# Optimization experiments

Hardware: AMD Instinct MI355X
Metric: run time of the kernel (lower is better)

## Reference

```python
import jax, jax.numpy as jnp
import numpy as np

N_NODES = 50000
N_EDGES = 400000
IN_DIM = 64
HID = 128
HEADS = 4
NEG_SLOPE = 0.2


def gat_conv(x, src, dst, W, a_src, a_dst, b, heads, out_ch, concat):
    N = x.shape[0]
    h = (x @ W).reshape(N, heads, out_ch)                 # [N,H,C]
    alpha_s = jnp.einsum('nhc,hc->nh', h, a_src)          # [N,H]
    alpha_d = jnp.einsum('nhc,hc->nh', h, a_dst)
    e = jax.nn.leaky_relu(alpha_s[src] + alpha_d[dst], NEG_SLOPE)  # [E,H]
    m = jax.ops.segment_max(e, dst, num_segments=N)
    m = jnp.where(jnp.isfinite(m), m, 0.0)
    ex = jnp.exp(e - m[dst])
    s = jax.ops.segment_sum(ex, dst, num_segments=N)
    alpha = ex / s[dst]                                   # segment softmax over incoming edges
    out = jax.ops.segment_sum(h[src] * alpha[:, :, None], dst, num_segments=N)  # [N,H,C]
    out = out.reshape(N, heads * out_ch) if concat else out.mean(axis=1)
    return out + b


def setup_inputs() -> dict:
    key = jax.random.key(0)
    ks = jax.random.split(key, 20)
    g = lambda i, shape, sc: (jax.random.normal(ks[i], shape, jnp.float32) * sc)
    x = g(0, (N_NODES, IN_DIM), 1.0)
    edge_index = jax.random.randint(ks[1], (2, N_EDGES), 0, N_NODES, dtype=jnp.int32)
    d = {
        'x': x, 'edge_index': edge_index,
        'W1': g(2, (IN_DIM, HEADS * HID), 0.1), 'a_src1': g(3, (HEADS, HID), 0.1), 'a_dst1': g(4, (HEADS, HID), 0.1), 'b1': jnp.zeros((HEADS * HID,), jnp.float32),
        'W2': g(5, (HEADS * HID, HEADS * HID), 0.05), 'a_src2': g(6, (HEADS, HID), 0.1), 'a_dst2': g(7, (HEADS, HID), 0.1), 'b2': jnp.zeros((HEADS * HID,), jnp.float32),
        'W3': g(8, (HEADS * HID, HID), 0.05), 'a_src3': g(9, (1, HID), 0.1), 'a_dst3': g(10, (1, HID), 0.1), 'b3': jnp.zeros((HID,), jnp.float32),
        'fc1_w': g(11, (HID, HID // 2), 0.1), 'fc1_b': jnp.zeros((HID // 2,), jnp.float32),
        'fc2_w': g(12, (HID // 2, 1), 0.1), 'fc2_b': jnp.zeros((1,), jnp.float32),
    }
    return d


def reference(x, edge_index, W1, a_src1, a_dst1, b1, W2, a_src2, a_dst2, b2, W3, a_src3, a_dst3, b3, fc1_w, fc1_b, fc2_w, fc2_b):
    N = x.shape[0]
    loop = jnp.arange(N, dtype=edge_index.dtype)
    src = jnp.concatenate([edge_index[0], loop])  # PyG GATConv adds self-loops by default
    dst = jnp.concatenate([edge_index[1], loop])
    h = jax.nn.elu(gat_conv(x, src, dst, W1, a_src1, a_dst1, b1, HEADS, HID, True))
    h = jax.nn.elu(gat_conv(h, src, dst, W2, a_src2, a_dst2, b2, HEADS, HID, True))
    h = jax.nn.elu(gat_conv(h, src, dst, W3, a_src3, a_dst3, b3, 1, HID, False))
    h = jax.nn.relu(h @ fc1_w + fc1_b)
    return jax.nn.sigmoid(h @ fc2_w + fc2_b)  # [N, 1]
```

## Files before the change

### kernel.cpp

```cpp
#include <hip/hip_runtime.h>
#include <math.h>

typedef __attribute__((ext_vector_type(8))) short short8;
typedef __attribute__((ext_vector_type(4))) float f32x4;
typedef unsigned short u16;
typedef unsigned int u32;

__device__ inline u16 f2b(float f) {
  u32 u = __float_as_uint(f);
  return (u16)((u + 0x7FFFu + ((u >> 16) & 1u)) >> 16);
}
__device__ inline float b2f(u16 b) { return __uint_as_float((u32)b << 16); }
__device__ inline float lrelu(float v) { return v > 0.f ? v : 0.2f * v; }
__device__ inline float elu1(float v) { return v > 0.f ? v : __expf(v) - 1.f; }

__device__ inline void gld_lds16(const void* g, void* l) {
  __builtin_amdgcn_global_load_lds((const __attribute__((address_space(1))) void*)g,
                                   (__attribute__((address_space(3))) void*)l, 16, 0, 0);
}

__global__ void fused_prep(const float* __restrict__ x, u16* __restrict__ xb, int NX,
                           const float* __restrict__ W1, u16* __restrict__ Wt1,
                           const float* __restrict__ W2, u16* __restrict__ Wt2,
                           const float* __restrict__ W3, u16* __restrict__ Wt3,
                           const int* __restrict__ ei, int E0, int ET,
                           int* __restrict__ deg) {
  int i = blockIdx.x * blockDim.x + threadIdx.x;
  if (i < NX) {
    xb[i] = f2b(x[i]);
    return;
  }
  i -= NX;
  if (i < 64 * 512) {
    int k = i / 512, n = i % 512;
    Wt1[n * 64 + k] = f2b(W1[i]);
    return;
  }
  i -= 64 * 512;
  if (i < 512 * 512) {
    int k = i / 512, n = i % 512;
    Wt2[n * 512 + k] = f2b(W2[i]);
    return;
  }
  i -= 512 * 512;
  if (i < 512 * 128) {
    int k = i / 128, n = i % 128;
    Wt3[n * 512 + k] = f2b(W3[i]);
    return;
  }
  i -= 512 * 128;
  if (i < ET) {
    int d = (i < E0) ? ei[E0 + i] : (i - E0);
    atomicAdd(&deg[d], 1);
  }
}

__global__ __launch_bounds__(256) void gemm_bf16_gat(
    const u16* __restrict__ A, const u16* __restrict__ Bt, u16* __restrict__ Hb,
    const float* __restrict__ a_src, const float* __restrict__ a_dst,
    float* __restrict__ aS, float* __restrict__ aD, int M, int HC, int K, int Hh,
    int gy, int nStrips) {
  int mIdx, nIdx;
  if (nStrips == 4) {
    int l = blockIdx.x;
    int xcd = l & 7, k = l >> 3;
    nIdx = k & 3;
    mIdx = xcd + 8 * (k >> 2);
    if (mIdx >= gy) return;
  } else {
    mIdx = blockIdx.x;
    nIdx = 0;
  }
  __shared__ u16 As[128 * 32];
  __shared__ u16 Bs[128 * 32];
  __shared__ float sRed[2][2][128];
  const int tid = threadIdx.x;
  const int w = tid >> 6, lane = tid & 63;
  const int wm = w >> 1, wn = w & 1;
  const int q = lane >> 4, l15 = lane & 15;
  const int nBase = nIdx * 128;
  const int mBase = mIdx * 128;
  const int h = nBase >> 7;
  const int srow = lane >> 2;
  const int skc = (lane & 3) * 8;

  f32x4 acc[4][4];
#pragma unroll
  for (int i = 0; i < 4; ++i)
#pragma unroll
    for (int j = 0; j < 4; ++j) acc[i][j] = (f32x4){0.f, 0.f, 0.f, 0.f};

  for (int k0 = 0; k0 < K; k0 += 32) {
#pragma unroll
    for (int r = 0; r < 2; ++r) {
      int lrow = w * 32 + r * 16 + srow;
      int ga = mBase + lrow;
      if (ga >= M) ga = M - 1;
      gld_lds16(A + (size_t)ga * K + k0 + skc, &As[(w * 32 + r * 16) * 32]);
      int gb = nBase + lrow;
      gld_lds16(Bt + (size_t)gb * K + k0 + skc, &Bs[(w * 32 + r * 16) * 32]);
    }
    __syncthreads();
    short8 af[4], bf[4];
#pragma unroll
    for (int i = 0; i < 4; ++i)
      af[i] = *(const short8*)&As[(wm * 64 + i * 16 + l15) * 32 + q * 8];
#pragma unroll
    for (int j = 0; j < 4; ++j)
      bf[j] = *(const short8*)&Bs[(wn * 64 + j * 16 + l15) * 32 + q * 8];
#pragma unroll
    for (int i = 0; i < 4; ++i)
#pragma unroll
      for (int j = 0; j < 4; ++j)
        acc[i][j] = __builtin_amdgcn_mfma_f32_16x16x32_bf16(af[i], bf[j], acc[i][j], 0, 0, 0);
    __syncthreads();
  }

  float asv[4], adv[4];
#pragma unroll
  for (int j = 0; j < 4; ++j) {
    int cw = wn * 64 + j * 16 + l15;
    asv[j] = a_src[h * 128 + cw];
    adv[j] = a_dst[h * 128 + cw];
  }
#pragma unroll
  for (int mi = 0; mi < 4; ++mi) {
#pragma unroll
    for (int r = 0; r < 4; ++r) {
      int row = mBase + wm * 64 + mi * 16 + q * 4 + r;
      float s = 0.f, d = 0.f;
#pragma unroll
      for (int j = 0; j < 4; ++j) {
        float v = acc[mi][j][r];
        s = fmaf(v, asv[j], s);
        d = fmaf(v, adv[j], d);
        if (row < M) Hb[(size_t)row * HC + nBase + wn * 64 + j * 16 + l15] = f2b(v);
      }
#pragma unroll
      for (int o = 8; o; o >>= 1) {
        s += __shfl_xor(s, o);
        d += __shfl_xor(d, o);
      }
      if (l15 == 0) {
        int lr = wm * 64 + mi * 16 + q * 4 + r;
        sRed[0][wn][lr] = s;
        sRed[1][wn][lr] = d;
      }
    }
  }
  __syncthreads();
  if (tid < 128) {
    int row = mBase + tid;
    if (row < M) {
      aS[(size_t)row * Hh + h] = sRed[0][0][tid] + sRed[0][1][tid];
      aD[(size_t)row * Hh + h] = sRed[1][0][tid] + sRed[1][1][tid];
    }
  }
}

__global__ __launch_bounds__(256) void scan_chunk(const int* __restrict__ deg,
                                                  int* __restrict__ incl,
                                                  int* __restrict__ bsums, int N) {
  __shared__ int sdata[256];
  const int t = threadIdx.x;
  const int base = blockIdx.x * 2048;
  int v[8];
  int sum = 0;
#pragma unroll
  for (int i = 0; i < 8; ++i) {
    int idx = base + t * 8 + i;
    v[i] = (idx < N) ? deg[idx] : 0;
    sum += v[i];
  }
  sdata[t] = sum;
  __syncthreads();
  for (int off = 1; off < 256; off <<= 1) {
    int x = (t >= off) ? sdata[t - off] : 0;
    __syncthreads();
    sdata[t] += x;
    __syncthreads();
  }
  int run = (t > 0) ? sdata[t - 1] : 0;
#pragma unroll
  for (int i = 0; i < 8; ++i) {
    int idx = base + t * 8 + i;
    run += v[i];
    if (idx < N) incl[idx] = run;
  }
  if (t == 255) bsums[blockIdx.x] = sdata[255];
}

__global__ void scan_final(const int* __restrict__ incl, const int* __restrict__ bsums,
                           int* __restrict__ rowptr, int N, int nb) {
  int i = blockIdx.x * blockDim.x + threadIdx.x;
  if (i >= N) return;
  int chunk = i >> 11;
  int pre = 0;
  for (int j = 0; j < chunk; ++j) pre += bsums[j];
  rowptr[i + 1] = incl[i] + pre;
  if (i == 0) rowptr[0] = 0;
}

__global__ void csr_fill(const int* __restrict__ ei, int E0, int ET,
                         const int* __restrict__ rowptr, int* __restrict__ cnt,
                         int* __restrict__ csr_src, int* __restrict__ csr_dst) {
  int e = blockIdx.x * blockDim.x + threadIdx.x;
  if (e >= ET) return;
  int s, d;
  if (e < E0) { s = ei[e]; d = ei[E0 + e]; }
  else        { s = e - E0; d = e - E0; }
  int pos = atomicAdd(&cnt[d], 1);
  csr_src[rowptr[d] + pos] = s;
  csr_dst[rowptr[d] + pos] = d;
}

__global__ __launch_bounds__(256) void edge_logits(const int* __restrict__ csr_src,
                                                   const int* __restrict__ csr_dst,
                                                   const float* __restrict__ aS,
                                                   const float* __restrict__ aD,
                                                   float* __restrict__ elog, int ET,
                                                   int Hh) {
  int e = blockIdx.x * blockDim.x + threadIdx.x;
  if (e >= ET) return;
  int s = csr_src[e], d = csr_dst[e];
  if (Hh == 4) {
    float4 a = *(const float4*)&aS[(size_t)s * 4];
    float4 b = *(const float4*)&aD[(size_t)d * 4];
    float4 r;
    r.x = lrelu(a.x + b.x);
    r.y = lrelu(a.y + b.y);
    r.z = lrelu(a.z + b.z);
    r.w = lrelu(a.w + b.w);
    *(float4*)&elog[(size_t)e * 4] = r;
  } else {
    elog[e] = lrelu(aS[s] + aD[d]);
  }
}

#define ACC8(A, pv, wgt)                                             \
  A[0] = fmaf(wgt, __uint_as_float(pv.x << 16), A[0]);               \
  A[1] = fmaf(wgt, __uint_as_float(pv.x & 0xffff0000u), A[1]);       \
  A[2] = fmaf(wgt, __uint_as_float(pv.y << 16), A[2]);               \
  A[3] = fmaf(wgt, __uint_as_float(pv.y & 0xffff0000u), A[3]);       \
  A[4] = fmaf(wgt, __uint_as_float(pv.z << 16), A[4]);               \
  A[5] = fmaf(wgt, __uint_as_float(pv.z & 0xffff0000u), A[5]);       \
  A[6] = fmaf(wgt, __uint_as_float(pv.w << 16), A[6]);               \
  A[7] = fmaf(wgt, __uint_as_float(pv.w & 0xffff0000u), A[7]);

__global__ __launch_bounds__(256) void gat_fused_agg(
    const int* __restrict__ rowptr, const int* __restrict__ csr_src,
    const u16* __restrict__ Hb, const float* __restrict__ elog,
    const float* __restrict__ bias, u16* __restrict__ outB,
    float* __restrict__ outF, int N) {
  const int wid = (int)((blockIdx.x * (blockDim.x >> 6)) + (threadIdx.x >> 6));
  const int lane = threadIdx.x & 63;
  if (wid >= N) return;
  const int beg = rowptr[wid];
  const int deg = rowptr[wid + 1] - beg;

  const int h = lane >> 4;
  const int e16 = lane & 15;
  const int c0 = lane * 8;
  const int hbase = lane & 48;
  float acc[8] = {};

  if (deg <= 16) {
    int srcv = 0;
    float l = -1e30f;
    if (e16 < deg) {
      srcv = csr_src[beg + e16];
      l = elog[(size_t)(beg + e16) * 4 + h];
    }
    uint4 pC[4];
#pragma unroll
    for (int j = 0; j < 4; ++j)
      if (j < deg) {
        int s = __shfl(srcv, j);
        pC[j] = *(const uint4*)&Hb[(size_t)s * 512 + c0];
      }
    float m = l;
#pragma unroll
    for (int o = 8; o; o >>= 1) m = fmaxf(m, __shfl_xor(m, o));
    float pexp = (e16 < deg) ? __expf(l - m) : 0.f;
    float cs = pexp;
#pragma unroll
    for (int o = 8; o; o >>= 1) cs += __shfl_xor(cs, o);
    pexp *= (1.f / cs);
    int e = 0;
    for (; e + 4 < deg; e += 4) {
      uint4 pN[4];
      int rem = deg - e - 4;
#pragma unroll
      for (int j = 0; j < 4; ++j)
        if (j < rem) {
          int s = __shfl(srcv, e + 4 + j);
          pN[j] = *(const uint4*)&Hb[(size_t)s * 512 + c0];
        }
#pragma unroll
      for (int j = 0; j < 4; ++j) {
        float wgt = __shfl(pexp, hbase | (e + j));
        ACC8(acc, pC[j], wgt)
      }
#pragma unroll
      for (int j = 0; j < 4; ++j) pC[j] = pN[j];
    }
#pragma unroll
    for (int j = 0; j < 4; ++j)
      if (j < deg - e) {
        float wgt = __shfl(pexp, hbase | (e + j));
        ACC8(acc, pC[j], wgt)
      }
  } else {
    float m = -1e30f, ssum = 0.f;
    for (int c = 0; c < deg; c += 16) {
      const int ce = min(16, deg - c);
      int srcv = 0;
      float l = -1e30f;
      if (e16 < ce) {
        srcv = csr_src[beg + c + e16];
        l = elog[(size_t)(beg + c + e16) * 4 + h];
      }
      float cm = l;
#pragma unroll
      for (int o = 8; o; o >>= 1) cm = fmaxf(cm, __shfl_xor(cm, o));
      float pexp, cs;
      if (c == 0) {
        m = cm;
        pexp = __expf(l - m);
        cs = pexp;
#pragma unroll
        for (int o = 8; o; o >>= 1) cs += __shfl_xor(cs, o);
        ssum = cs;
      } else {
        float newm = fmaxf(m, cm);
        float r = __expf(m - newm);
        m = newm;
        pexp = __expf(l - m);
        cs = pexp;
#pragma unroll
        for (int o = 8; o; o >>= 1) cs += __shfl_xor(cs, o);
        ssum = ssum * r + cs;
#pragma unroll
        for (int i = 0; i < 8; ++i) acc[i] *= r;
      }
      int e = 0;
      for (; e + 4 <= ce; e += 4) {
        int se0 = __shfl(srcv, e + 0), se1 = __shfl(srcv, e + 1);
        int se2 = __shfl(srcv, e + 2), se3 = __shfl(srcv, e + 3);
        float w0 = __shfl(pexp, hbase | (e + 0)), w1 = __shfl(pexp, hbase | (e + 1));
        float w2 = __shfl(pexp, hbase | (e + 2)), w3 = __shfl(pexp, hbase | (e + 3));
        uint4 p0 = *(const uint4*)&Hb[(size_t)se0 * 512 + c0];
        uint4 p1 = *(const uint4*)&Hb[(size_t)se1 * 512 + c0];
        uint4 p2 = *(const uint4*)&Hb[(size_t)se2 * 512 + c0];
        uint4 p3 = *(const uint4*)&Hb[(size_t)se3 * 512 + c0];
        ACC8(acc, p0, w0)
        ACC8(acc, p1, w1)
        ACC8(acc, p2, w2)
        ACC8(acc, p3, w3)
      }
      for (; e < ce; ++e) {
        int se = __shfl(srcv, e);
        float wgt = __shfl(pexp, hbase | e);
        uint4 pv = *(const uint4*)&Hb[(size_t)se * 512 + c0];
        ACC8(acc, pv, wgt)
      }
    }
    const float inv = 1.f / ssum;
#pragma unroll
    for (int i = 0; i < 8; ++i) acc[i] *= inv;
  }

  float bv[8];
  *(float4*)&bv[0] = *(const float4*)&bias[c0];
  *(float4*)&bv[4] = *(const float4*)&bias[c0 + 4];
  u16 packed[8];
#pragma unroll
  for (int i = 0; i < 8; ++i) {
    float v = elu1(acc[i] + bv[i]);
    acc[i] = v;
    packed[i] = f2b(v);
  }
  if (outB) *(uint4*)&outB[(size_t)wid * 512 + c0] = *(const uint4*)packed;
  if (outF) {
    *(float4*)&outF[(size_t)wid * 512 + c0] = make_float4(acc[0], acc[1], acc[2], acc[3]);
    *(float4*)&outF[(size_t)wid * 512 + c0 + 4] =
        make_float4(acc[4], acc[5], acc[6], acc[7]);
  }
}

__global__ __launch_bounds__(256) void gat_agg_h1(
    const int* __restrict__ rowptr, const int* __restrict__ csr_src,
    const u16* __restrict__ Hb, const float* __restrict__ elog,
    const float* __restrict__ bias, float* __restrict__ outF, int N) {
  const int wid = (int)((blockIdx.x * (blockDim.x >> 6)) + (threadIdx.x >> 6));
  const int lane = threadIdx.x & 63;
  if (wid >= N) return;
  const int beg = rowptr[wid];
  const int deg = rowptr[wid + 1] - beg;
  const int g = lane & 15;
  const int es = lane >> 4;
  const int c0 = g * 8;
  float acc[8] = {};

  if (deg <= 64) {
    int srcv = 0;
    float l = -1e30f;
    if (lane < deg) {
      srcv = csr_src[beg + lane];
      l = elog[beg + lane];
    }
    const int dm1 = deg - 1;
    uint4 pC;
    {
      int s = __shfl(srcv, min(es, dm1));
      pC = *(const uint4*)&Hb[(size_t)s * 128 + c0];
    }
    float m = l;
#pragma unroll
    for (int o = 32; o; o >>= 1) m = fmaxf(m, __shfl_xor(m, o));
    float pexp = (lane < deg) ? __expf(l - m) : 0.f;
    float cs = pexp;
#pragma unroll
    for (int o = 32; o; o >>= 1) cs += __shfl_xor(cs, o);
    pexp *= (1.f / cs);
    int t = 0;
    for (; t + 4 < deg; t += 4) {
      uint4 pN;
      {
        int s = __shfl(srcv, min(t + 4 + es, dm1));
        pN = *(const uint4*)&Hb[(size_t)s * 128 + c0];
      }
      float w = __shfl(pexp, t + es);
      ACC8(acc, pC, w)
      pC = pN;
    }
    {
      int idx = t + es;
      float w = __shfl(pexp, min(idx, dm1));
      if (idx > dm1) w = 0.f;
      ACC8(acc, pC, w)
    }
  } else {
    float m = -1e30f, ssum = 0.f;
    for (int c = 0; c < deg; c += 64) {
      const int ce = min(64, deg - c);
      int srcv = 0;
      float l = -1e30f;
      if (lane < ce) {
        srcv = csr_src[beg + c + lane];
        l = elog[beg + c + lane];
      }
      float cm = l;
#pragma unroll
      for (int o = 32; o; o >>= 1) cm = fmaxf(cm, __shfl_xor(cm, o));
      float pexp, cs;
      if (c == 0) {
        m = cm;
        pexp = __expf(l - m);
        cs = pexp;
#pragma unroll
        for (int o = 32; o; o >>= 1) cs += __shfl_xor(cs, o);
        ssum = cs;
      } else {
        float newm = fmaxf(m, cm);
        float r = __expf(m - newm);
        m = newm;
        pexp = __expf(l - m);
        cs = pexp;
#pragma unroll
        for (int o = 32; o; o >>= 1) cs += __shfl_xor(cs, o);
        ssum = ssum * r + cs;
#pragma unroll
        for (int i = 0; i < 8; ++i) acc[i] *= r;
      }
      for (int t = 0; t < ce; t += 4) {
        int idx = t + es;
        int se = __shfl(srcv, idx & 63);
        float wgt = __shfl(pexp, idx & 63);
        if (idx < ce) {
          uint4 pv = *(const uint4*)&Hb[(size_t)se * 128 + c0];
          ACC8(acc, pv, wgt)
        }
      }
    }
    const float inv = 1.f / ssum;
#pragma unroll
    for (int i = 0; i < 8; ++i) acc[i] *= inv;
  }
#pragma unroll
  for (int i = 0; i < 8; ++i) {
    acc[i] += __shfl_xor(acc[i], 16);
    acc[i] += __shfl_xor(acc[i], 32);
  }
  if (lane < 16) {
    float o[8];
#pragma unroll
    for (int i = 0; i < 8; ++i) o[i] = elu1(acc[i] + bias[c0 + i]);
    *(float4*)&outF[(size_t)wid * 128 + c0] = make_float4(o[0], o[1], o[2], o[3]);
    *(float4*)&outF[(size_t)wid * 128 + c0 + 4] = make_float4(o[4], o[5], o[6], o[7]);
  }
}

__global__ __launch_bounds__(256) void fc_head(const float* __restrict__ A,
                                               const float* __restrict__ B,
                                               const float* __restrict__ bias,
                                               const float* __restrict__ w2,
                                               const float* __restrict__ b2,
                                               float* __restrict__ out, int M) {
  __shared__ float As[16][64];
  __shared__ float Bs[16][64];
  __shared__ float sP[64][17];
  const int tid = threadIdx.x;
  const int tx = tid & 15, ty = tid >> 4;
  const int mBase = blockIdx.y * 64;
  const int aRow = tid >> 2;
  const int aK = (tid & 3) << 2;
  const int bC = tid & 63;
  const int bR0 = tid >> 6;
  const int K = 128, N = 64;
  float acc[4][4] = {};
  for (int k0 = 0; k0 < K; k0 += 16) {
    float4 av = make_float4(0.f, 0.f, 0.f, 0.f);
    int gr = mBase + aRow;
    if (gr < M) av = *(const float4*)&A[(size_t)gr * K + k0 + aK];
    As[aK + 0][aRow] = av.x;
    As[aK + 1][aRow] = av.y;
    As[aK + 2][aRow] = av.z;
    As[aK + 3][aRow] = av.w;
#pragma unroll
    for (int i = 0; i < 4; ++i) {
      int r = bR0 + i * 4;
      Bs[r][bC] = B[(size_t)(k0 + r) * N + bC];
    }
    __syncthreads();
#pragma unroll
    for (int k = 0; k < 16; ++k) {
      float4 a = *(const float4*)&As[k][ty * 4];
      float4 b = *(const float4*)&Bs[k][tx * 4];
      float ar[4] = {a.x, a.y, a.z, a.w};
      float br[4] = {b.x, b.y, b.z, b.w};
#pragma unroll
      for (int i = 0; i < 4; ++i)
#pragma unroll
        for (int j = 0; j < 4; ++j) acc[i][j] = fmaf(ar[i], br[j], acc[i][j]);
    }
    __syncthreads();
  }
  float4 bv = *(const float4*)&bias[tx * 4];
  float4 wv = *(const float4*)&w2[tx * 4];
#pragma unroll
  for (int i = 0; i < 4; ++i) {
    float p = 0.f;
    p = fmaf(fmaxf(acc[i][0] + bv.x, 0.f), wv.x, p);
    p = fmaf(fmaxf(acc[i][1] + bv.y, 0.f), wv.y, p);
    p = fmaf(fmaxf(acc[i][2] + bv.z, 0.f), wv.z, p);
    p = fmaf(fmaxf(acc[i][3] + bv.w, 0.f), wv.w, p);
    sP[ty * 4 + i][tx] = p;
  }
  __syncthreads();
  if (tid < 64) {
    int row = mBase + tid;
    if (row < M) {
      float s = 0.f;
#pragma unroll
      for (int t = 0; t < 16; ++t) s += sP[tid][t];
      out[row] = 1.f / (1.f + expf(-(s + b2[0])));
    }
  }
}

extern "C" void kernel_launch(void* const* d_in, const int* in_sizes, int n_in,
                              void* d_out, int out_size, void* d_ws, size_t ws_size,
                              hipStream_t stream) {
  const float* x    = (const float*)d_in[0];
  const int*   ei   = (const int*)d_in[1];
  const float* W1   = (const float*)d_in[2];
  const float* as1  = (const float*)d_in[3];
  const float* ad1  = (const float*)d_in[4];
  const float* b1   = (const float*)d_in[5];
  const float* W2   = (const float*)d_in[6];
  const float* as2  = (const float*)d_in[7];
  const float* ad2  = (const float*)d_in[8];
  const float* b2   = (const float*)d_in[9];
  const float* W3   = (const float*)d_in[10];
  const float* as3  = (const float*)d_in[11];
  const float* ad3  = (const float*)d_in[12];
  const float* b3   = (const float*)d_in[13];
  const float* fc1w = (const float*)d_in[14];
  const float* fc1b = (const float*)d_in[15];
  const float* fc2w = (const float*)d_in[16];
  const float* fc2b = (const float*)d_in[17];
  float* out = (float*)d_out;

  const int N  = in_sizes[0] / 64;
  const int E0 = in_sizes[1] / 2;
  const int ET = E0 + N;

  char* ws = (char*)d_ws;
  size_t off = 0;
  auto alloc = [&](size_t bytes) -> void* {
    void* p = ws + off;
    off += (bytes + 255) & ~(size_t)255;
    return p;
  };
  u16*   bufXb   = (u16*)alloc((size_t)N * 512 * 2);
  u16*   bufHb   = (u16*)alloc((size_t)N * 512 * 2);
  float* bufF    = (float*)alloc((size_t)N * 128 * 4);
  float* aS      = (float*)alloc((size_t)N * 4 * 4);
  float* aD      = (float*)alloc((size_t)N * 4 * 4);
  u16*   Wt1     = (u16*)alloc((size_t)512 * 64 * 2);
  u16*   Wt2     = (u16*)alloc((size_t)512 * 512 * 2);
  u16*   Wt3     = (u16*)alloc((size_t)128 * 512 * 2);
  int*   degcnt  = (int*)alloc((size_t)2 * N * 4);
  int*   deg     = degcnt;
  int*   cnt     = degcnt + N;
  int*   incl    = (int*)alloc((size_t)N * 4);
  int*   rowptr  = (int*)alloc((size_t)(N + 1) * 4);
  int*   bsums   = (int*)alloc(256 * 4);
  int*   csr_src = (int*)alloc((size_t)ET * 4);
  int*   csr_dst = (int*)alloc((size_t)ET * 4);
  float* elog    = (float*)alloc((size_t)ET * 4 * 4);
  (void)ws_size; (void)n_in; (void)out_size;

  hipMemsetAsync(degcnt, 0, (size_t)2 * N * 4, stream);
  const int NX = N * 64;
  const int prepTotal = NX + 64 * 512 + 512 * 512 + 512 * 128 + ET;
  hipLaunchKernelGGL(fused_prep, dim3((prepTotal + 255) / 256), dim3(256), 0, stream, x,
                     bufXb, NX, W1, Wt1, W2, Wt2, W3, Wt3, ei, E0, ET, deg);

  int nb = (N + 2047) / 2048;
  hipLaunchKernelGGL(scan_chunk, dim3(nb), dim3(256), 0, stream, deg, incl, bsums, N);
  hipLaunchKernelGGL(scan_final, dim3((N + 255) / 256), dim3(256), 0, stream, incl, bsums,
                     rowptr, N, nb);
  int eb = (ET + 255) / 256;
  hipLaunchKernelGGL(csr_fill, dim3(eb), dim3(256), 0, stream, ei, E0, ET, rowptr, cnt,
                     csr_src, csr_dst);

  const int gy = (N + 127) / 128;
  const int grid4 = ((gy + 7) / 8) * 8 * 4;
  const int aggGrid = (N + 3) / 4;

  hipLaunchKernelGGL(gemm_bf16_gat, dim3(grid4), dim3(256), 0, stream, bufXb, Wt1, bufHb,
                     as1, ad1, aS, aD, N, 512, 64, 4, gy, 4);
  hipLaunchKernelGGL(edge_logits, dim3(eb), dim3(256), 0, stream, csr_src, csr_dst, aS,
                     aD, elog, ET, 4);
  hipLaunchKernelGGL(gat_fused_agg, dim3(aggGrid), dim3(256), 0, stream, rowptr,
                     csr_src, bufHb, elog, b1, bufXb, nullptr, N);
  hipLaunchKernelGGL(gemm_bf16_gat, dim3(grid4), dim3(256), 0, stream, bufXb, Wt2, bufHb,
                     as2, ad2, aS, aD, N, 512, 512, 4, gy, 4);
  hipLaunchKernelGGL(edge_logits, dim3(eb), dim3(256), 0, stream, csr_src, csr_dst, aS,
                     aD, elog, ET, 4);
  hipLaunchKernelGGL(gat_fused_agg, dim3(aggGrid), dim3(256), 0, stream, rowptr,
                     csr_src, bufHb, elog, b2, bufXb, nullptr, N);
  hipLaunchKernelGGL(gemm_bf16_gat, dim3(gy), dim3(256), 0, stream, bufXb, Wt3, bufHb,
                     as3, ad3, aS, aD, N, 128, 512, 1, gy, 1);
  hipLaunchKernelGGL(edge_logits, dim3(eb), dim3(256), 0, stream, csr_src, csr_dst, aS,
                     aD, elog, ET, 1);
  hipLaunchKernelGGL(gat_agg_h1, dim3(aggGrid), dim3(256), 0, stream, rowptr, csr_src,
                     bufHb, elog, b3, bufF, N);

  hipLaunchKernelGGL(fc_head, dim3(1, (N + 63) / 64), dim3(256), 0, stream, bufF, fc1w,
                     fc1b, fc2w, fc2b, out, N);
}
```

Baseline: 452.2 us.

## Reorder layer-1 GAT to aggregate raw 64-dim inputs before projection

For the first GAT layer, attention logits are now computed directly from x using precomputed W1·a_src/a_dst vectors, so the full projection is not needed for them. Aggregation runs over the 64-dim input features per head, and only then is the aggregated [N,4,64] tensor multiplied by W1 with a block-diagonal per-head GEMM that fuses bias and ELU. This removes gathering 512-wide bf16 rows per edge in layer 1, replacing them with 64-wide fp32 gathers. The cost is a larger intermediate buffer and a different rounding order for the bf16 output.

New measurement: 454.4 us. No clear change (+0.5%).

```diff
diff --git a/kernel.cpp b/kernel.cpp
--- a/kernel.cpp
+++ b/kernel.cpp
@@ -19,18 +19,12 @@
                                    (__attribute__((address_space(3))) void*)l, 16, 0, 0);
 }
 
-__global__ void fused_prep(const float* __restrict__ x, u16* __restrict__ xb, int NX,
-                           const float* __restrict__ W1, u16* __restrict__ Wt1,
+__global__ void fused_prep(const float* __restrict__ W1, u16* __restrict__ Wt1,
                            const float* __restrict__ W2, u16* __restrict__ Wt2,
                            const float* __restrict__ W3, u16* __restrict__ Wt3,
                            const int* __restrict__ ei, int E0, int ET,
                            int* __restrict__ deg) {
   int i = blockIdx.x * blockDim.x + threadIdx.x;
-  if (i < NX) {
-    xb[i] = f2b(x[i]);
-    return;
-  }
-  i -= NX;
   if (i < 64 * 512) {
     int k = i / 512, n = i % 512;
     Wt1[n * 64 + k] = f2b(W1[i]);
@@ -158,6 +152,74 @@
   }
 }
 
+__global__ __launch_bounds__(256) void gemm_bd_l1(
+    const u16* __restrict__ A, const u16* __restrict__ Bt,
+    const float* __restrict__ bias, u16* __restrict__ outB, int M, int gy) {
+  int l = blockIdx.x;
+  int xcd = l & 7, kk = l >> 3;
+  int nIdx = kk & 3;
+  int mIdx = xcd + 8 * (kk >> 2);
+  if (mIdx >= gy) return;
+  __shared__ u16 As[128 * 32];
+  __shared__ u16 Bs[128 * 32];
+  const int tid = threadIdx.x;
+  const int w = tid >> 6, lane = tid & 63;
+  const int wm = w >> 1, wn = w & 1;
+  const int q = lane >> 4, l15 = lane & 15;
+  const int nBase = nIdx * 128, mBase = mIdx * 128;
+  const int srow = lane >> 2, skc = (lane & 3) * 8;
+
+  f32x4 acc[4][4];
+#pragma unroll
+  for (int i = 0; i < 4; ++i)
+#pragma unroll
+    for (int j = 0; j < 4; ++j) acc[i][j] = (f32x4){0.f, 0.f, 0.f, 0.f};
+
+  for (int k0 = 0; k0 < 64; k0 += 32) {
+#pragma unroll
+    for (int r = 0; r < 2; ++r) {
+      int lrow = w * 32 + r * 16 + srow;
+      int ga = mBase + lrow;
+      if (ga >= M) ga = M - 1;
+      gld_lds16(A + (size_t)ga * 256 + nIdx * 64 + k0 + skc,
+                &As[(w * 32 + r * 16) * 32]);
+      int gb = nBase + lrow;
+      gld_lds16(Bt + (size_t)gb * 64 + k0 + skc, &Bs[(w * 32 + r * 16) * 32]);
+    }
+    __syncthreads();
+    short8 af[4], bf[4];
+#pragma unroll
+    for (int i = 0; i < 4; ++i)
+      af[i] = *(const short8*)&As[(wm * 64 + i * 16 + l15) * 32 + q * 8];
+#pragma unroll
+    for (int j = 0; j < 4; ++j)
+      bf[j] = *(const short8*)&Bs[(wn * 64 + j * 16 + l15) * 32 + q * 8];
+#pragma unroll
+    for (int i = 0; i < 4; ++i)
+#pragma unroll
+      for (int j = 0; j < 4; ++j)
+        acc[i][j] = __builtin_amdgcn_mfma_f32_16x16x32_bf16(af[i], bf[j], acc[i][j], 0, 0, 0);
+    __syncthreads();
+  }
+
+  float bvv[4];
+#pragma unroll
+  for (int j = 0; j < 4; ++j) bvv[j] = bias[nBase + wn * 64 + j * 16 + l15];
+#pragma unroll
+  for (int mi = 0; mi < 4; ++mi)
+#pragma unroll
+    for (int r = 0; r < 4; ++r) {
+      int row = mBase + wm * 64 + mi * 16 + q * 4 + r;
+      if (row < M) {
+#pragma unroll
+        for (int j = 0; j < 4; ++j) {
+          float v = elu1(acc[mi][j][r] + bvv[j]);
+          outB[(size_t)row * 512 + nBase + wn * 64 + j * 16 + l15] = f2b(v);
+        }
+      }
+    }
+}
+
 __global__ __launch_bounds__(256) void scan_chunk(const int* __restrict__ deg,
                                                   int* __restrict__ incl,
                                                   int* __restrict__ bsums, int N) {
@@ -212,6 +274,40 @@
   int pos = atomicAdd(&cnt[d], 1);
   csr_src[rowptr[d] + pos] = s;
   csr_dst[rowptr[d] + pos] = d;
+}
+
+__global__ void make_wsd(const float* __restrict__ W1, const float* __restrict__ as1,
+                         const float* __restrict__ ad1, float* __restrict__ wsd) {
+  int t = blockIdx.x * blockDim.x + threadIdx.x;
+  if (t >= 512) return;
+  int k = t >> 3, c8 = t & 7;
+  int h = c8 & 3;
+  const float* a = (c8 >= 4) ? ad1 : as1;
+  float s = 0.f;
+  for (int c = 0; c < 128; ++c) s += W1[k * 512 + h * 128 + c] * a[h * 128 + c];
+  wsd[k * 8 + c8] = s;
+}
+
+__global__ __launch_bounds__(256) void asad_x(const float* __restrict__ xf,
+                                              const float* __restrict__ wsd,
+                                              float* __restrict__ aS,
+                                              float* __restrict__ aD, int N) {
+  const int wid = (int)((blockIdx.x * (blockDim.x >> 6)) + (threadIdx.x >> 6));
+  const int lane = threadIdx.x & 63;
+  if (wid >= N) return;
+  float xv = xf[(size_t)wid * 64 + lane];
+  float4 w0 = *(const float4*)&wsd[lane * 8];
+  float4 w1 = *(const float4*)&wsd[lane * 8 + 4];
+  float s[8] = {xv * w0.x, xv * w0.y, xv * w0.z, xv * w0.w,
+                xv * w1.x, xv * w1.y, xv * w1.z, xv * w1.w};
+#pragma unroll
+  for (int i = 0; i < 8; ++i)
+#pragma unroll
+    for (int o = 32; o; o >>= 1) s[i] += __shfl_xor(s[i], o);
+  if (lane == 0) {
+    *(float4*)&aS[(size_t)wid * 4] = make_float4(s[0], s[1], s[2], s[3]);
+    *(float4*)&aD[(size_t)wid * 4] = make_float4(s[4], s[5], s[6], s[7]);
+  }
 }
 
 __global__ __launch_bounds__(256) void edge_logits(const int* __restrict__ csr_src,
@@ -235,6 +331,115 @@
   } else {
     elog[e] = lrelu(aS[s] + aD[d]);
   }
+}
+
+__global__ __launch_bounds__(256) void gat_agg_x(
+    const int* __restrict__ rowptr, const int* __restrict__ csr_src,
+    const float* __restrict__ xf, const float* __restrict__ elog,
+    u16* __restrict__ aggB, int N) {
+  const int wid = (int)((blockIdx.x * (blockDim.x >> 6)) + (threadIdx.x >> 6));
+  const int lane = threadIdx.x & 63;
+  if (wid >= N) return;
+  const int beg = rowptr[wid];
+  const int deg = rowptr[wid + 1] - beg;
+  const int h = lane >> 4;
+  const int e16 = lane & 15;
+  float acc[4] = {};
+
+  if (deg <= 16) {
+    int srcv = 0;
+    float l = -1e30f;
+    if (e16 < deg) {
+      srcv = csr_src[beg + e16];
+      l = elog[(size_t)(beg + e16) * 4 + h];
+    }
+    float xv[16];
+#pragma unroll
+    for (int j = 0; j < 16; ++j)
+      if (j < deg) {
+        int s = __shfl(srcv, j);
+        xv[j] = xf[(size_t)s * 64 + lane];
+      }
+    float m = l;
+#pragma unroll
+    for (int o = 8; o; o >>= 1) m = fmaxf(m, __shfl_xor(m, o));
+    float pexp = (e16 < deg) ? __expf(l - m) : 0.f;
+    float cs = pexp;
+#pragma unroll
+    for (int o = 8; o; o >>= 1) cs += __shfl_xor(cs, o);
+    pexp *= (1.f / cs);
+#pragma unroll
+    for (int j = 0; j < 16; ++j)
+      if (j < deg) {
+        float w0 = __shfl(pexp, j);
+        float w1 = __shfl(pexp, 16 | j);
+        float w2 = __shfl(pexp, 32 | j);
+        float w3 = __shfl(pexp, 48 | j);
+        acc[0] = fmaf(w0, xv[j], acc[0]);
+        acc[1] = fmaf(w1, xv[j], acc[1]);
+        acc[2] = fmaf(w2, xv[j], acc[2]);
+        acc[3] = fmaf(w3, xv[j], acc[3]);
+      }
+  } else {
+    float m = -1e30f, ssum = 0.f;
+    for (int c = 0; c < deg; c += 16) {
+      const int ce = min(16, deg - c);
+      int srcv = 0;
+      float l = -1e30f;
+      if (e16 < ce) {
+        srcv = csr_src[beg + c + e16];
+        l = elog[(size_t)(beg + c + e16) * 4 + h];
+      }
+      float xv[16];
+#pragma unroll
+      for (int j = 0; j < 16; ++j)
+        if (j < ce) {
+          int s = __shfl(srcv, j);
+          xv[j] = xf[(size_t)s * 64 + lane];
+        }
+      float cm = l;
+#pragma unroll
+      for (int o = 8; o; o >>= 1) cm = fmaxf(cm, __shfl_xor(cm, o));
+      float pexp, cs;
+      if (c == 0) {
+        m = cm;
+        pexp = (e16 < ce) ? __expf(l - m) : 0.f;
+        cs = pexp;
+#pragma unroll
+        for (int o = 8; o; o >>= 1) cs += __shfl_xor(cs, o);
+        ssum = cs;
+      } else {
+        float newm = fmaxf(m, cm);
+        float r = __expf(m - newm);
+        m = newm;
+        pexp = (e16 < ce) ? __expf(l - m) : 0.f;
+        cs = pexp;
+#pragma unroll
+        for (int o = 8; o; o >>= 1) cs += __shfl_xor(cs, o);
+        ssum = ssum * r + cs;
+#pragma unroll
+        for (int i = 0; i < 4; ++i) acc[i] *= r;
+      }
+#pragma unroll
+      for (int j = 0; j < 16; ++j)
+        if (j < ce) {
+          float w0 = __shfl(pexp, j);
+          float w1 = __shfl(pexp, 16 | j);
+          float w2 = __shfl(pexp, 32 | j);
+          float w3 = __shfl(pexp, 48 | j);
+          acc[0] = fmaf(w0, xv[j], acc[0]);
+          acc[1] = fmaf(w1, xv[j], acc[1]);
+          acc[2] = fmaf(w2, xv[j], acc[2]);
+          acc[3] = fmaf(w3, xv[j], acc[3]);
+        }
+    }
+    const float inv = 1.f / ssum;
+#pragma unroll
+    for (int i = 0; i < 4; ++i) acc[i] *= inv;
+  }
+#pragma unroll
+  for (int hh = 0; hh < 4; ++hh)
+    aggB[((size_t)wid * 4 + hh) * 64 + lane] = f2b(acc[hh]);
 }
 
 #define ACC8(A, pv, wgt)                                             \
@@ -611,6 +816,8 @@
   u16*   Wt1     = (u16*)alloc((size_t)512 * 64 * 2);
   u16*   Wt2     = (u16*)alloc((size_t)512 * 512 * 2);
   u16*   Wt3     = (u16*)alloc((size_t)128 * 512 * 2);
+  u16*   aggB    = (u16*)alloc((size_t)N * 256 * 2);
+  float* wsd     = (float*)alloc((size_t)64 * 8 * 4);
   int*   degcnt  = (int*)alloc((size_t)2 * N * 4);
   int*   deg     = degcnt;
   int*   cnt     = degcnt + N;
@@ -623,10 +830,9 @@
   (void)ws_size; (void)n_in; (void)out_size;
 
   hipMemsetAsync(degcnt, 0, (size_t)2 * N * 4, stream);
-  const int NX = N * 64;
-  const int prepTotal = NX + 64 * 512 + 512 * 512 + 512 * 128 + ET;
-  hipLaunchKernelGGL(fused_prep, dim3((prepTotal + 255) / 256), dim3(256), 0, stream, x,
-                     bufXb, NX, W1, Wt1, W2, Wt2, W3, Wt3, ei, E0, ET, deg);
+  const int prepTotal = 64 * 512 + 512 * 512 + 512 * 128 + ET;
+  hipLaunchKernelGGL(fused_prep, dim3((prepTotal + 255) / 256), dim3(256), 0, stream,
+                     W1, Wt1, W2, Wt2, W3, Wt3, ei, E0, ET, deg);
 
   int nb = (N + 2047) / 2048;
   hipLaunchKernelGGL(scan_chunk, dim3(nb), dim3(256), 0, stream, deg, incl, bsums, N);
@@ -640,18 +846,22 @@
   const int grid4 = ((gy + 7) / 8) * 8 * 4;
   const int aggGrid = (N + 3) / 4;
 
-  hipLaunchKernelGGL(gemm_bf16_gat, dim3(grid4), dim3(256), 0, stream, bufXb, Wt1, bufHb,
-                     as1, ad1, aS, aD, N, 512, 64, 4, gy, 4);
+  hipLaunchKernelGGL(make_wsd, dim3(2), dim3(256), 0, stream, W1, as1, ad1, wsd);
+  hipLaunchKernelGGL(asad_x, dim3(aggGrid), dim3(256), 0, stream, x, wsd, aS, aD, N);
   hipLaunchKernelGGL(edge_logits, dim3(eb), dim3(256), 0, stream, csr_src, csr_dst, aS,
                      aD, elog, ET, 4);
-  hipLaunchKernelGGL(gat_fused_agg, dim3(aggGrid), dim3(256), 0, stream, rowptr,
-                     csr_src, bufHb, elog, b1, bufXb, nullptr, N);
+  hipLaunchKernelGGL(gat_agg_x, dim3(aggGrid), dim3(256), 0, stream, rowptr, csr_src, x,
+                     elog, aggB, N);
+  hipLaunchKernelGGL(gemm_bd_l1, dim3(grid4), dim3(256), 0, stream, aggB, Wt1, b1,
+                     bufXb, N, gy);
+
   hipLaunchKernelGGL(gemm_bf16_gat, dim3(grid4), dim3(256), 0, stream, bufXb, Wt2, bufHb,
                      as2, ad2, aS, aD, N, 512, 512, 4, gy, 4);
   hipLaunchKernelGGL(edge_logits, dim3(eb), dim3(256), 0, stream, csr_src, csr_dst, aS,
                      aD, elog, ET, 4);
   hipLaunchKernelGGL(gat_fused_agg, dim3(aggGrid), dim3(256), 0, stream, rowptr,
                      csr_src, bufHb, elog, b2, bufXb, nullptr, N);
+
   hipLaunchKernelGGL(gemm_bf16_gat, dim3(gy), dim3(256), 0, stream, bufXb, Wt3, bufHb,
                      as3, ad3, aS, aD, N, 128, 512, 1, gy, 1);
   hipLaunchKernelGGL(edge_logits, dim3(eb), dim3(256), 0, stream, csr_src, csr_dst, aS,
```
